# Performance work log

Hardware: AMD Instinct MI355X
Metric: run time of the kernel (lower is better)

## Reference

```python
import jax, jax.numpy as jnp
import numpy as np

R = 32            # voxel resolution
ALPHA = 0.1       # LeakyReLU slope
BN_EPS = 1e-4     # BatchNormalization epsilon
VOX_EPS = 1e-6    # Voxelization eps (normalize=True)


def _bn_train(x, gamma, beta, axes):
    # training-mode batch norm over `axes`, channel axis = 1
    mean = jnp.mean(x, axes, keepdims=True)
    var = jnp.var(x, axes, keepdims=True)
    bshape = (1, -1) + (1,) * (x.ndim - 2)
    return gamma.reshape(bshape) * (x - mean) * jax.lax.rsqrt(var + BN_EPS) + beta.reshape(bshape)


def _lrelu(x):
    return jnp.where(x >= 0, x, ALPHA * x)


def _voxelize(features, coords):
    # features [B,C,N], coords [B,3,N] -> grid [B,C,R,R,R], norm_coords [B,3,N] in [0,R-1]
    centered = coords - jnp.mean(coords, axis=2, keepdims=True)
    max_norm = jnp.max(jnp.linalg.norm(centered, axis=1, keepdims=True), axis=2, keepdims=True)
    norm = centered / (max_norm * 2.0 + VOX_EPS) + 0.5
    norm = jnp.clip(norm * R, 0.0, R - 1)
    vox = jnp.round(norm).astype(jnp.int32)              # [B,3,N]
    flat = (vox[:, 0] * R + vox[:, 1]) * R + vox[:, 2]   # [B,N]

    def per_batch(f, idx):  # f [C,N], idx [N]
        sums = jax.ops.segment_sum(f.T, idx, num_segments=R ** 3)            # [R^3,C]
        cnt = jax.ops.segment_sum(jnp.ones_like(idx, f.dtype), idx, num_segments=R ** 3)
        return (sums / jnp.maximum(cnt, 1.0)[:, None]).T                      # [C,R^3]

    grid = jax.vmap(per_batch)(features, flat)            # [B,C,R^3]
    B, C = features.shape[0], features.shape[1]
    return grid.reshape(B, C, R, R, R), norm


def _conv3d(x, w, b):
    # x [B,C,D,H,W], w [k,k,k,Cin,Cout], 'same' padding
    y = jax.lax.conv_general_dilated(x, w, (1, 1, 1), 'SAME',
                                     dimension_numbers=('NCDHW', 'DHWIO', 'NCDHW'))
    return y + b.reshape(1, -1, 1, 1, 1)


def _trilinear_devoxelize(vf, coords):
    # vf [B,C,R^3], coords [B,3,N] in [0,R-1] -> [B,C,N]
    c0f = jnp.clip(jnp.floor(coords), 0.0, R - 1)
    frac = coords - c0f                                   # [B,3,N]
    c0 = c0f.astype(jnp.int32)
    c1 = jnp.minimum(c0 + 1, R - 1)
    out = jnp.zeros((vf.shape[0], vf.shape[1], coords.shape[2]), vf.dtype)
    for dx in (0, 1):
        for dy in (0, 1):
            for dz in (0, 1):
                xs = c1[:, 0] if dx else c0[:, 0]
                ys = c1[:, 1] if dy else c0[:, 1]
                zs = c1[:, 2] if dz else c0[:, 2]
                w = ((frac[:, 0] if dx else 1 - frac[:, 0]) *
                     (frac[:, 1] if dy else 1 - frac[:, 1]) *
                     (frac[:, 2] if dz else 1 - frac[:, 2]))           # [B,N]
                idx = (xs * R + ys) * R + zs                            # [B,N]
                g = jnp.take_along_axis(vf, idx[:, None, :], axis=2)    # [B,C,N]
                out = out + w[:, None, :] * g
    return out


def setup_inputs() -> dict:
    key = jax.random.key(0)
    ks = jax.random.split(key, 16)
    B, C, N, K = 8, 64, 16384, 3
    s = 0.05
    return {
        'features': jax.random.normal(ks[0], (B, C, N), jnp.float32),
        'coords': jax.random.normal(ks[1], (B, 3, N), jnp.float32),
        'conv1_w': jax.random.normal(ks[2], (K, K, K, C, C), jnp.float32) * s,
        'conv1_b': jnp.zeros((C,), jnp.float32),
        'bn1_gamma': jnp.ones((C,), jnp.float32),
        'bn1_beta': jnp.zeros((C,), jnp.float32),
        'conv2_w': jax.random.normal(ks[3], (K, K, K, C, C), jnp.float32) * s,
        'conv2_b': jnp.zeros((C,), jnp.float32),
        'bn2_gamma': jnp.ones((C,), jnp.float32),
        'bn2_beta': jnp.zeros((C,), jnp.float32),
        'pf_w': jax.random.normal(ks[4], (C, C), jnp.float32) * s,
        'pf_bias': jnp.zeros((C,), jnp.float32),
        'pf_gamma': jnp.ones((C,), jnp.float32),
        'pf_beta': jnp.zeros((C,), jnp.float32),
    }


def reference(features, coords, conv1_w, conv1_b, bn1_gamma, bn1_beta,
              conv2_w, conv2_b, bn2_gamma, bn2_beta,
              pf_w, pf_bias, pf_gamma, pf_beta):
    vgrid, norm_coords = _voxelize(features, coords)
    v = _lrelu(_bn_train(_conv3d(vgrid, conv1_w, conv1_b), bn1_gamma, bn1_beta, (0, 2, 3, 4)))
    v = _lrelu(_bn_train(_conv3d(v, conv2_w, conv2_b), bn2_gamma, bn2_beta, (0, 2, 3, 4)))
    vflat = v.reshape(v.shape[0], v.shape[1], -1)                 # [B,C,R^3]
    vpts = _trilinear_devoxelize(vflat, norm_coords)              # [B,C,N]
    # point branch: shared MLP (1x1 conv) + BN + LeakyReLU
    p = jnp.einsum('bcn,cd->bdn', features, pf_w) + pf_bias[None, :, None]
    p = _lrelu(_bn_train(p, pf_gamma, pf_beta, (0, 2)))
    return vpts + p, coords
```

## Files before the change

### kernel.cpp

```cpp
#include <hip/hip_runtime.h>
#include <stdint.h>

#define RR 32
#define R3 32768
#define NB 8
#define NCH 64
#define NP 16384

typedef unsigned short u16;
typedef uint32_t u32;
typedef __attribute__((ext_vector_type(8))) short bf8;
typedef __attribute__((ext_vector_type(4))) float f4;
typedef __attribute__((ext_vector_type(16))) float f16x;

#define MFMA(a,b,c)   __builtin_amdgcn_mfma_f32_16x16x32_bf16(a,b,c,0,0,0)
#define MFMA32(a,b,c) __builtin_amdgcn_mfma_f32_32x32x16_bf16(a,b,c,0,0,0)

__device__ __forceinline__ float bf2f(u16 v){
  union { u32 u; float f; } x; x.u = ((u32)v) << 16; return x.f;
}
__device__ __forceinline__ float u2f(u32 u){
  union { u32 u; float f; } x; x.u = u; return x.f;
}
__device__ __forceinline__ u16 f2bf(float f){
  union { float f; u32 u; } x; x.f = f;
  u32 r = x.u + 0x7fffu + ((x.u >> 16) & 1u);
  return (u16)(r >> 16);
}
__device__ __forceinline__ float ldf(const void* p, size_t i, int isbf){
  return isbf ? bf2f(((const u16*)p)[i]) : ((const float*)p)[i];
}

#define OFF_GRID  0ull
#define OFF_BUF1  33554432ull
#define OFF_FT    33554432ull
#define OFF_P     67108864ull
#define OFF_CNT   83886080ull
#define OFF_SMALL 84934656ull
#define OFF_STAT  84936704ull
#define OFF_OFFS  84948992ull
#define OFF_NC    85997568ull
#define OFF_VIDX  87570432ull
#define OFF_SORT  88094720ull
#define OFF_WF1   88619008ull
#define OFF_WF2   88840192ull
#define OFF_WFP   89061376ull
#define WS_NEED   89069568ull
#define ZOFF      OFF_CNT
#define ZBYTES    1062912ull

__global__ void k_dtype(const uint32_t* __restrict__ gamma_raw, int* __restrict__ flag){
  if (threadIdx.x == 0) *flag = (gamma_raw[0] == 0x3F800000u) ? 0 : 1;
}

__global__ void k_coordstats(const void* __restrict__ coords, float* __restrict__ small,
                             const int* __restrict__ dflag){
  int b = blockIdx.x; int tid = threadIdx.x;
  int isbf = *dflag;
  __shared__ float red[1024];
  size_t cb = (size_t)b*3*NP;
  float sx=0.f, sy=0.f, sz=0.f;
  for (int n = tid; n < NP; n += 1024){
    sx += ldf(coords, cb+n, isbf);
    sy += ldf(coords, cb+NP+n, isbf);
    sz += ldf(coords, cb+2*NP+n, isbf);
  }
  float m[3]; float* sums[3] = {&sx,&sy,&sz};
  for (int a = 0; a < 3; a++){
    red[tid] = *sums[a]; __syncthreads();
    for (int s = 512; s > 0; s >>= 1){ if (tid < s) red[tid] += red[tid+s]; __syncthreads(); }
    m[a] = red[0] * (1.0f/NP); __syncthreads();
  }
  float vm = 0.f;
  for (int n = tid; n < NP; n += 1024){
    float cx = ldf(coords, cb+n, isbf)      - m[0];
    float cy = ldf(coords, cb+NP+n, isbf)   - m[1];
    float cz = ldf(coords, cb+2*NP+n, isbf) - m[2];
    vm = fmaxf(vm, sqrtf(cx*cx + cy*cy + cz*cz));
  }
  red[tid] = vm; __syncthreads();
  for (int s = 512; s > 0; s >>= 1){ if (tid < s) red[tid] = fmaxf(red[tid], red[tid+s]); __syncthreads(); }
  if (tid == 0){
    small[384 + b*4 + 0] = m[0];
    small[384 + b*4 + 1] = m[1];
    small[384 + b*4 + 2] = m[2];
    small[384 + b*4 + 3] = 1.0f / (2.0f*red[0] + 1e-6f);
  }
}

__global__ void k_pointprep(const void* __restrict__ coords, const float* __restrict__ small,
                            float* __restrict__ nc, int* __restrict__ vidx, int* __restrict__ cnt,
                            const int* __restrict__ dflag){
  int g = blockIdx.x*256 + threadIdx.x;
  int isbf = *dflag;
  int b = g >> 14; int n = g & (NP-1);
  float mx = small[384+b*4+0], my = small[384+b*4+1], mz = small[384+b*4+2], sc = small[384+b*4+3];
  size_t cb = (size_t)b*3*NP;
  float nx = ((ldf(coords, cb+n, isbf)      - mx)*sc + 0.5f) * 32.0f;
  float ny = ((ldf(coords, cb+NP+n, isbf)   - my)*sc + 0.5f) * 32.0f;
  float nz = ((ldf(coords, cb+2*NP+n, isbf) - mz)*sc + 0.5f) * 32.0f;
  nx = fminf(fmaxf(nx, 0.f), 31.f);
  ny = fminf(fmaxf(ny, 0.f), 31.f);
  nz = fminf(fmaxf(nz, 0.f), 31.f);
  nc[(b*3+0)*NP + n] = nx; nc[(b*3+1)*NP + n] = ny; nc[(b*3+2)*NP + n] = nz;
  int vx = (int)rintf(nx), vy = (int)rintf(ny), vz = (int)rintf(nz);
  int flat = (vx*32 + vy)*32 + vz;
  vidx[g] = flat;
  atomicAdd(&cnt[b*R3 + flat], 1);
}

__global__ void k_scan(const int* __restrict__ cnt, int* __restrict__ off){
  __shared__ int part[1024];
  int b = blockIdx.x, tid = threadIdx.x;
  int base = b*R3 + tid*32;
  int s = 0;
  for (int i = 0; i < 32; i++) s += cnt[base + i];
  part[tid] = s; __syncthreads();
  for (int st = 1; st < 1024; st <<= 1){
    int v = (tid >= st) ? part[tid - st] : 0;
    __syncthreads();
    part[tid] += v;
    __syncthreads();
  }
  int run = (tid == 0) ? 0 : part[tid - 1];
  for (int i = 0; i < 32; i++){ off[base + i] = run; run += cnt[base + i]; }
}

__global__ void k_sortpts(const int* __restrict__ vidx, int* __restrict__ off, int* __restrict__ sorted){
  int g = blockIdx.x*256 + threadIdx.x;
  int b = g >> 14; int n = g & (NP-1);
  int v = vidx[g];
  int slot = atomicAdd(&off[b*R3 + v], 1);
  sorted[b*NP + slot] = n;
}

__global__ __launch_bounds__(256) void k_voxsum(const u16* __restrict__ fT, const int* __restrict__ sorted,
                         const int* __restrict__ cnt, const int* __restrict__ off,
                         u16* __restrict__ grid){
  int wid = blockIdx.x*4 + (threadIdx.x >> 6);
  int lane = threadIdx.x & 63;
  int b = wid >> 11;
  int v0 = (wid & 2047) << 4;
  int base = b*R3 + v0;
  int c = 0, e = 0;
  if (lane < 16){ c = cnt[base + lane]; e = off[base + lane]; }
  int start = __shfl(e - c, 0);
  int total = __shfl(e, 15) - start;
  const int* sb = sorted + (size_t)b*NP;
  int sp = 0;
  if (lane < total) sp = sb[start + lane];
  #pragma unroll
  for (int i = 0; i < 16; i++){
    int ci = __shfl(c, i);
    int rel = __shfl(e, i) - ci - start;
    float a0 = 0.f, a1 = 0.f;
    int j = 0;
    for (; j + 1 < ci; j += 2){
      int k0 = rel + j, k1 = k0 + 1;
      int n0 = (k0 < 64) ? __shfl(sp, k0) : sb[start + k0];
      int n1 = (k1 < 64) ? __shfl(sp, k1) : sb[start + k1];
      a0 += bf2f(fT[((size_t)(b*NP + n0))*64 + lane]);
      a1 += bf2f(fT[((size_t)(b*NP + n1))*64 + lane]);
    }
    if (j < ci){
      int k0 = rel + j;
      int n0 = (k0 < 64) ? __shfl(sp, k0) : sb[start + k0];
      a0 += bf2f(fT[((size_t)(b*NP + n0))*64 + lane]);
    }
    float acc = a0 + a1;
    grid[((size_t)(base + i))*64 + lane] = f2bf(acc / (float)max(ci, 1));
  }
}

__global__ void k_wprep(const void* __restrict__ w, u16* __restrict__ wfrag, const int* __restrict__ dflag){
  int idx = blockIdx.x; int lane = threadIdx.x;
  int isbf = *dflag;
  int ntl = idx & 3; int kk = (idx >> 2) & 1; int tap = idx >> 3;
  int lh = lane & 15, quad = lane >> 4;
  int n = ntl*16 + lh;
  u16* dst = wfrag + ((size_t)idx*64 + lane)*8;
  for (int j = 0; j < 8; j++){
    int k = kk*32 + quad*8 + j;
    dst[j] = f2bf(ldf(w, (size_t)(tap*64 + k)*64 + n, isbf));
  }
}

__global__ void k_wprep32(const void* __restrict__ w, u16* __restrict__ wfrag, const int* __restrict__ dflag){
  int idx = blockIdx.x; int lane = threadIdx.x;
  int isbf = *dflag;
  int nh = idx & 1; int ks = (idx >> 1) & 3; int tap = idx >> 3;
  int n = nh*32 + (lane & 31);
  int khalf = lane >> 5;
  u16* dst = wfrag + ((size_t)idx*64 + lane)*8;
  for (int j = 0; j < 8; j++){
    int cin = ks*16 + khalf*8 + j;
    dst[j] = f2bf(ldf(w, (size_t)(tap*64 + cin)*64 + n, isbf));
  }
}

__device__ __forceinline__ void bn_params(const float* __restrict__ spread, int c, float invM,
                                          float* mean, float* rs){
  float su = 0.f, sq = 0.f;
  #pragma unroll
  for (int i = 0; i < 8; i++){ su += spread[i*128 + c]; sq += spread[i*128 + 64 + c]; }
  float m = su * invM;
  *mean = m;
  *rs = rsqrtf(sq*invM - m*m + 1e-4f);
}

#define ISSUE_W(BANK, TAP) do { \
  _Pragma("unroll") \
  for (int ks_ = 0; ks_ < 4; ks_++) \
    BANK[ks_] = *(const bf8*)(wstream + (size_t)((TAP)*4 + ks_)*1024); \
} while(0)

#define ISSUE_A8(BANK, TAP, H) do { \
  const int t_ = (TAP); \
  const int dwi_ = t_ % 3, dvi_ = (t_/3) % 3, dui_ = t_/9; \
  const u16* rp0_ = &lds_in[((2*(H) + dui_)*6 + vsel + dvi_)*2176]; \
  const u16* rp1_ = rp0_ + 6*2176; \
  const int wp_ = mlane + dwi_; \
  const int wb_ = wp_*64, wx_ = wp_ & 7; \
  _Pragma("unroll") \
  for (int ks_ = 0; ks_ < 4; ks_++){ \
    const int off_ = wb_ + ((((ks_*2) + khalf) ^ wx_) << 3); \
    BANK[ks_]     = *(const bf8*)(rp0_ + off_); \
    BANK[4 + ks_] = *(const bf8*)(rp1_ + off_); \
  } \
} while(0)

#define CONSUME(BW, BA, ACC0, ACC1) do { \
  _Pragma("unroll") \
  for (int ks_ = 0; ks_ < 4; ks_++){ \
    ACC0 = MFMA32(BA[ks_],     BW[ks_], ACC0); \
    ACC1 = MFMA32(BA[4 + ks_], BW[ks_], ACC1); \
  } \
} while(0)

template<int BN>
__global__ __launch_bounds__(512, 1) void k_conv_t(const u16* __restrict__ in, const u16* __restrict__ wfrag,
                                                   u16* __restrict__ out, const float* __restrict__ spread,
                                                   const void* __restrict__ gamma, const void* __restrict__ beta,
                                                   const int* __restrict__ dflag){
  __shared__ u16 lds_in[36*2176];
  __shared__ float bnA[64], bnB[64];
  int bx = blockIdx.x;
  int b = bx >> 6; int r = bx & 63;
  int u0 = (r >> 3) * 4; int v0 = (r & 7) * 4;
  int tid = threadIdx.x, wv = tid >> 6, lane = tid & 63;

  if constexpr (BN){
    if (tid < 64){
      int isbf = *dflag;
      float mean, rs;
      bn_params(spread, tid, 1.0f/(NB*R3), &mean, &rs);
      float ga = ldf(gamma, tid, isbf), be = ldf(beta, tid, isbf);
      float A = ga*rs;
      bnA[tid] = A; bnB[tid] = be - mean*A;
    }
    __syncthreads();
  }

  uint4 zz; zz.x = 0; zz.y = 0; zz.z = 0; zz.w = 0;
  for (int ri = wv; ri < 36; ri += 8){
    int u2 = u0 + (ri / 6) - 1;
    int v2 = v0 + (ri % 6) - 1;
    uint4* dstrow = (uint4*)&lds_in[ri*2176];
    if ((unsigned)u2 > 31u || (unsigned)v2 > 31u){
      for (int i = lane; i < 272; i += 64) dstrow[i] = zz;
      continue;
    }
    const uint4* src = (const uint4*)(in + ((size_t)(b*R3 + (u2*32 + v2)*32))*64);
    if (lane < 8) dstrow[lane] = zz;
    else if (lane < 16) dstrow[264 + (lane & 7)] = zz;
    #pragma unroll
    for (int ch = 0; ch < 4; ch++){
      int idx = ch*64 + lane;
      int w = idx >> 3, cc = idx & 7;
      uint4 v = src[idx];
      if constexpr (BN){
        u32 in4[4] = {v.x, v.y, v.z, v.w};
        u32 o4[4];
        #pragma unroll
        for (int k = 0; k < 4; k++){
          int c = cc*8 + 2*k;
          float lo = u2f(in4[k] << 16);
          float hi = u2f(in4[k] & 0xFFFF0000u);
          lo = bnA[c]*lo + bnB[c];     lo = (lo >= 0.f) ? lo : 0.1f*lo;
          hi = bnA[c+1]*hi + bnB[c+1]; hi = (hi >= 0.f) ? hi : 0.1f*hi;
          o4[k] = (u32)f2bf(lo) | ((u32)f2bf(hi) << 16);
        }
        v.x = o4[0]; v.y = o4[1]; v.z = o4[2]; v.w = o4[3];
      }
      int wp = w + 1;
      dstrow[wp*8 + (cc ^ (wp & 7))] = v;
    }
  }
  __syncthreads();

  int vsel = wv & 3, nh = wv >> 2;
  int v_i = v0 + vsel;
  int mlane = lane & 31;
  int khalf = lane >> 5;
  f16x acc0, acc1, acc2, acc3;
  #pragma unroll
  for (int i = 0; i < 16; i++){ acc0[i] = 0.f; acc1[i] = 0.f; acc2[i] = 0.f; acc3[i] = 0.f; }

  const u16* wstream = wfrag + (size_t)nh*512 + (size_t)lane*8;

  bf8 W0[4], W1[4], W2[4];
  bf8 Aa[8], Ab[8];

  ISSUE_W(W0, 0);
  ISSUE_W(W1, 1);
  ISSUE_A8(Aa, 0, 0);

  #pragma unroll
  for (int tap = 0; tap < 27; ++tap){
    const int pf = tap + 2;
    if (pf < 27){
      if (pf % 3 == 0)      ISSUE_W(W0, pf);
      else if (pf % 3 == 1) ISSUE_W(W1, pf);
      else                  ISSUE_W(W2, pf);
    }
    ISSUE_A8(Ab, tap, 1);
    __builtin_amdgcn_sched_barrier(0);
    if (tap < 25)       asm volatile("s_waitcnt vmcnt(8) lgkmcnt(8)");
    else if (tap == 25) asm volatile("s_waitcnt vmcnt(4) lgkmcnt(8)");
    else                asm volatile("s_waitcnt vmcnt(0) lgkmcnt(8)");
    __builtin_amdgcn_sched_barrier(0);
    {
      const int wsel = tap % 3;
      if (wsel == 0)      CONSUME(W0, Aa, acc0, acc1);
      else if (wsel == 1) CONSUME(W1, Aa, acc0, acc1);
      else                CONSUME(W2, Aa, acc0, acc1);
    }
    if (tap + 1 < 27) ISSUE_A8(Aa, tap + 1, 0);
    __builtin_amdgcn_sched_barrier(0);
    if (tap < 25)       asm volatile("s_waitcnt vmcnt(8) lgkmcnt(8)");
    else if (tap == 25) asm volatile("s_waitcnt vmcnt(4) lgkmcnt(8)");
    else                asm volatile("s_waitcnt vmcnt(0) lgkmcnt(0)");
    __builtin_amdgcn_sched_barrier(0);
    {
      const int wsel = tap % 3;
      if (wsel == 0)      CONSUME(W0, Ab, acc2, acc3);
      else if (wsel == 1) CONSUME(W1, Ab, acc2, acc3);
      else                CONSUME(W2, Ab, acc2, acc3);
    }
  }

  int co = nh*32 + mlane;
  int rbase = 4*khalf;
  size_t base0 = ((size_t)(b*R3 + ((u0+0)*32 + v_i)*32))*64;
  size_t base1 = ((size_t)(b*R3 + ((u0+1)*32 + v_i)*32))*64;
  size_t base2 = ((size_t)(b*R3 + ((u0+2)*32 + v_i)*32))*64;
  size_t base3 = ((size_t)(b*R3 + ((u0+3)*32 + v_i)*32))*64;
  #pragma unroll
  for (int reg = 0; reg < 16; reg++){
    int row = (reg & 3) + 8*(reg >> 2) + rbase;
    out[base0 + (size_t)row*64 + co] = f2bf(acc0[reg]);
    out[base1 + (size_t)row*64 + co] = f2bf(acc1[reg]);
    out[base2 + (size_t)row*64 + co] = f2bf(acc2[reg]);
    out[base3 + (size_t)row*64 + co] = f2bf(acc3[reg]);
  }
}

__global__ __launch_bounds__(256) void k_stats2(const u16* __restrict__ buf, float* __restrict__ spread, int M){
  __shared__ float sred[4*128];
  int tid = threadIdx.x, bx = blockIdx.x;
  int wv = tid >> 6, lane = tid & 63;
  int sub = lane & 7;
  int g = bx*256 + tid;
  float s[8], s2[8];
  #pragma unroll
  for (int j = 0; j < 8; j++){ s[j] = 0.f; s2[j] = 0.f; }
  const uint4* p4 = (const uint4*)buf;
  size_t total = (size_t)M * 8;
  for (size_t f = g; f < total; f += 262144){
    uint4 v = p4[f];
    u32 ws_[4] = {v.x, v.y, v.z, v.w};
    #pragma unroll
    for (int k = 0; k < 4; k++){
      float lo = u2f(ws_[k] << 16);
      float hi = u2f(ws_[k] & 0xFFFF0000u);
      s[2*k]   += lo; s2[2*k]   += lo*lo;
      s[2*k+1] += hi; s2[2*k+1] += hi*hi;
    }
  }
  #pragma unroll
  for (int j = 0; j < 8; j++){
    #pragma unroll
    for (int m = 8; m <= 32; m <<= 1){
      s[j]  += __shfl_xor(s[j],  m);
      s2[j] += __shfl_xor(s2[j], m);
    }
  }
  if (lane < 8){
    #pragma unroll
    for (int j = 0; j < 8; j++){
      sred[wv*128 + sub*8 + j]      = s[j];
      sred[wv*128 + 64 + sub*8 + j] = s2[j];
    }
  }
  __syncthreads();
  if (tid < 128){
    float t = sred[tid] + sred[128+tid] + sred[256+tid] + sred[384+tid];
    atomicAdd(&spread[(bx & 7)*128 + tid], t);
  }
}

__global__ __launch_bounds__(256) void k_ftrans(const void* __restrict__ feat, u16* __restrict__ fT,
                                                const int* __restrict__ dflag){
  __shared__ u16 t[64*72];
  int bx = blockIdx.x;
  int isbf = *dflag;
  int b = bx >> 8; int n0 = (bx & 255) * 64;
  int tid = threadIdx.x;
  int c = tid >> 2, q = tid & 3;
  if (isbf){
    const uint4* src = (const uint4*)((const u16*)feat + ((size_t)(b*NCH + c))*NP + n0 + q*16);
    uint4 v0 = src[0], v1 = src[1];
    *(uint4*)&t[c*72 + q*16]     = v0;
    *(uint4*)&t[c*72 + q*16 + 8] = v1;
  } else {
    const float4* src = (const float4*)((const float*)feat + ((size_t)(b*NCH + c))*NP + n0 + q*16);
    #pragma unroll
    for (int h = 0; h < 4; h++){
      float4 f = src[h];
      u16* d = &t[c*72 + q*16 + h*4];
      d[0] = f2bf(f.x); d[1] = f2bf(f.y); d[2] = f2bf(f.z); d[3] = f2bf(f.w);
    }
  }
  __syncthreads();
  int n = tid >> 2, qc = tid & 3;
  union { u16 h[16]; uint4 v[2]; } pk;
  #pragma unroll
  for (int j = 0; j < 16; j++) pk.h[j] = t[(qc*16 + j)*72 + n];
  uint4* dst = (uint4*)(fT + ((size_t)(b*NP + n0 + n))*64 + qc*16);
  dst[0] = pk.v[0]; dst[1] = pk.v[1];
}

__global__ void k_pgemm(const u16* __restrict__ fT, const u16* __restrict__ wfp, u16* __restrict__ p){
  __shared__ u16 As[128*64];
  int bx = blockIdx.x;
  size_t row0 = (size_t)bx * 128;
  int tid = threadIdx.x, wv = tid >> 6, lane = tid & 63;
  const uint4* src = (const uint4*)(fT + row0*64);
  uint4* dst = (uint4*)As;
  for (int i = tid; i < 1024; i += 256) dst[i] = src[i];
  __syncthreads();
  int lh = lane & 15, quad = lane >> 4;
  f4 z4 = {0.f,0.f,0.f,0.f};
  f4 acc[2][4];
  for (int i = 0; i < 2; i++) for (int j = 0; j < 4; j++) acc[i][j] = z4;
  const u16* ap = &As[(wv*32)*64];
  #pragma unroll
  for (int kk = 0; kk < 2; kk++){
    bf8 a0 = *(const bf8*)(ap + lh*64 + kk*32 + quad*8);
    bf8 a1 = *(const bf8*)(ap + (16+lh)*64 + kk*32 + quad*8);
    #pragma unroll
    for (int ntl = 0; ntl < 4; ntl++){
      bf8 bf = *(const bf8*)(wfp + ((size_t)(kk*4 + ntl)*64 + lane)*8);
      acc[0][ntl] = MFMA(a0, bf, acc[0][ntl]);
      acc[1][ntl] = MFMA(a1, bf, acc[1][ntl]);
    }
  }
  #pragma unroll
  for (int mt = 0; mt < 2; mt++)
    for (int ntl = 0; ntl < 4; ntl++)
      for (int reg = 0; reg < 4; reg++){
        int rr = wv*32 + mt*16 + quad*4 + reg;
        p[(row0 + rr)*64 + ntl*16 + lh] = f2bf(acc[mt][ntl][reg]);
      }
}

__global__ void k_devox(const u16* __restrict__ grid, const u16* __restrict__ p,
                        const float* __restrict__ stP, const float* __restrict__ st2,
                        const void* __restrict__ pfg, const void* __restrict__ pfb,
                        const void* __restrict__ g2, const void* __restrict__ b2,
                        const float* __restrict__ nc, void* __restrict__ out0,
                        const int* __restrict__ dflag){
  __shared__ float t[64*65];
  int bx = blockIdx.x;
  int isbf = *dflag;
  int b = bx >> 8; int n0 = (bx & 255) * 64;
  int tid = threadIdx.x, wv = tid >> 6, lane = tid & 63;
  int c = lane;
  float meanP, rsP;
  bn_params(stP, c, 1.0f/(NB*NP), &meanP, &rsP);
  float gaP = ldf(pfg, c, isbf), beP = ldf(pfb, c, isbf);
  float mean2, rs2;
  bn_params(st2, c, 1.0f/(NB*R3), &mean2, &rs2);
  float ga2 = ldf(g2, c, isbf), be2 = ldf(b2, c, isbf);
  float A2 = ga2*rs2, B2 = be2 - mean2*A2;
  for (int pt = wv; pt < 64; pt += 4){
    int n = n0 + pt;
    float nx = nc[(b*3+0)*NP + n];
    float ny = nc[(b*3+1)*NP + n];
    float nz = nc[(b*3+2)*NP + n];
    float x0f = floorf(nx), y0f = floorf(ny), z0f = floorf(nz);
    int x0 = (int)x0f, y0 = (int)y0f, z0 = (int)z0f;
    float fx = nx - x0f, fy = ny - y0f, fz = nz - z0f;
    int x1 = min(x0+1,31), y1 = min(y0+1,31), z1 = min(z0+1,31);
    float acc = 0.f;
    #pragma unroll
    for (int k = 0; k < 8; k++){
      int dx = k >> 2, dy = (k >> 1) & 1, dz = k & 1;
      int xs = dx ? x1 : x0, ys = dy ? y1 : y0, zs = dz ? z1 : z0;
      float wgt = (dx ? fx : 1.f-fx)*(dy ? fy : 1.f-fy)*(dz ? fz : 1.f-fz);
      float gv = bf2f(grid[((size_t)(b*R3 + (xs*32+ys)*32 + zs))*64 + c]);
      gv = A2*gv + B2;
      gv = (gv >= 0.f) ? gv : 0.1f*gv;
      acc += wgt * gv;
    }
    float pv = bf2f(p[((size_t)(b*NP + n))*64 + c]);
    float y = gaP*(pv - meanP)*rsP + beP;
    y = (y >= 0.f) ? y : 0.1f*y;
    t[pt*65 + c] = acc + y;
  }
  __syncthreads();
  for (int cp = 0; cp < 16; cp++){
    int co = wv + cp*4;
    size_t oi = ((size_t)(b*NCH + co))*NP + n0 + lane;
    float val = t[lane*65 + co];
    if (isbf) ((u16*)out0)[oi] = f2bf(val);
    else      ((float*)out0)[oi] = val;
  }
}

__global__ void k_copycoords(const void* __restrict__ coords, void* __restrict__ out0,
                             const int* __restrict__ dflag){
  int g = blockIdx.x*256 + threadIdx.x;
  int isbf = *dflag;
  size_t oi = (size_t)NB*NCH*NP + g;
  if (isbf) ((u16*)out0)[oi]   = ((const u16*)coords)[g];
  else      ((float*)out0)[oi] = ((const float*)coords)[g];
}

extern "C" void kernel_launch(void* const* d_in, const int* in_sizes, int n_in,
                              void* d_out, int out_size, void* d_ws, size_t ws_size,
                              hipStream_t stream){
  if (ws_size < WS_NEED) return;

  const void* feat   = d_in[0];
  const void* coords = d_in[1];
  const void* w1     = d_in[2];
  const void* g1     = d_in[4];
  const void* b1     = d_in[5];
  const void* w2     = d_in[6];
  const void* g2     = d_in[8];
  const void* b2     = d_in[9];
  const void* pw     = d_in[10];
  const void* pg     = d_in[12];
  const void* pb     = d_in[13];

  char* ws = (char*)d_ws;
  u16*   gridv = (u16*)(ws + OFF_GRID);
  u16*   buf1  = (u16*)(ws + OFF_BUF1);
  u16*   fT    = (u16*)(ws + OFF_FT);
  u16*   p     = (u16*)(ws + OFF_P);
  int*   cnt   = (int*)(ws + OFF_CNT);
  float* small = (float*)(ws + OFF_SMALL);
  int*   dflag = (int*)(small + 448);
  float* stat  = (float*)(ws + OFF_STAT);
  int*   offs  = (int*)(ws + OFF_OFFS);
  float* nc    = (float*)(ws + OFF_NC);
  int*   vidx  = (int*)(ws + OFF_VIDX);
  int*   sorted= (int*)(ws + OFF_SORT);
  u16*   wf1   = (u16*)(ws + OFF_WF1);
  u16*   wf2   = (u16*)(ws + OFF_WF2);
  u16*   wfp   = (u16*)(ws + OFF_WFP);

  hipMemsetAsync(ws + ZOFF, 0, ZBYTES, stream);
  k_dtype<<<1, 64, 0, stream>>>((const uint32_t*)g1, dflag);

  k_wprep32<<<27*8, 64, 0, stream>>>(w1, wf1, dflag);
  k_wprep32<<<27*8, 64, 0, stream>>>(w2, wf2, dflag);
  k_wprep<<<8, 64, 0, stream>>>(pw, wfp, dflag);

  k_coordstats<<<NB, 1024, 0, stream>>>(coords, small, dflag);
  k_pointprep<<<NB*NP/256, 256, 0, stream>>>(coords, small, nc, vidx, cnt, dflag);
  k_scan<<<NB, 1024, 0, stream>>>(cnt, offs);
  k_sortpts<<<NB*NP/256, 256, 0, stream>>>(vidx, offs, sorted);

  k_ftrans<<<NB*NP/64, 256, 0, stream>>>(feat, fT, dflag);
  k_voxsum<<<NB*R3/64, 256, 0, stream>>>(fT, sorted, cnt, offs, gridv);
  k_pgemm<<<NB*NP/128, 256, 0, stream>>>(fT, wfp, p);
  k_stats2<<<1024, 256, 0, stream>>>(p, stat + 2048, NB*NP);

  k_conv_t<0><<<NB*64, 512, 0, stream>>>(gridv, wf1, buf1, nullptr, nullptr, nullptr, nullptr);
  k_stats2<<<1024, 256, 0, stream>>>(buf1, stat + 0, NB*R3);

  k_conv_t<1><<<NB*64, 512, 0, stream>>>(buf1, wf2, gridv, stat + 0, g1, b1, dflag);
  k_stats2<<<1024, 256, 0, stream>>>(gridv, stat + 1024, NB*R3);

  k_devox<<<NB*NP/64, 256, 0, stream>>>(gridv, p, stat + 2048, stat + 1024,
                                        pg, pb, g2, b2, nc, d_out, dflag);
  k_copycoords<<<NB*3*NP/256, 256, 0, stream>>>(coords, d_out, dflag);
}
```

Baseline: 391.4 us.

## Fuse BN statistics into conv epilogues and coords copy into pointprep

The conv kernels now reduce per-channel sum and sum-of-squares from their fp32 accumulators and atomically add them into a spread stats buffer. This removes the two separate k_stats2 passes that reread each conv output from memory. The coordinate passthrough copy moves into k_pointprep, which drops one more launch. Statistics now come from fp32 values rather than bf16-rounded outputs, and the added atomics could contend on the 8-way spread slots.

```diff
diff --git a/kernel.cpp b/kernel.cpp
--- a/kernel.cpp
+++ b/kernel.cpp
@@ -90,12 +90,20 @@
 
 __global__ void k_pointprep(const void* __restrict__ coords, const float* __restrict__ small,
                             float* __restrict__ nc, int* __restrict__ vidx, int* __restrict__ cnt,
-                            const int* __restrict__ dflag){
+                            void* __restrict__ out0, const int* __restrict__ dflag){
   int g = blockIdx.x*256 + threadIdx.x;
   int isbf = *dflag;
   int b = g >> 14; int n = g & (NP-1);
   float mx = small[384+b*4+0], my = small[384+b*4+1], mz = small[384+b*4+2], sc = small[384+b*4+3];
   size_t cb = (size_t)b*3*NP;
+  size_t ob = (size_t)NB*NCH*NP + cb + n;
+  if (isbf){
+    const u16* cs = (const u16*)coords; u16* o = (u16*)out0;
+    o[ob] = cs[cb+n]; o[ob+NP] = cs[cb+NP+n]; o[ob+2*NP] = cs[cb+2*NP+n];
+  } else {
+    const float* cs = (const float*)coords; float* o = (float*)out0;
+    o[ob] = cs[cb+n]; o[ob+NP] = cs[cb+NP+n]; o[ob+2*NP] = cs[cb+2*NP+n];
+  }
   float nx = ((ldf(coords, cb+n, isbf)      - mx)*sc + 0.5f) * 32.0f;
   float ny = ((ldf(coords, cb+NP+n, isbf)   - my)*sc + 0.5f) * 32.0f;
   float nz = ((ldf(coords, cb+2*NP+n, isbf) - mz)*sc + 0.5f) * 32.0f;
@@ -240,6 +248,7 @@
 template<int BN>
 __global__ __launch_bounds__(512, 1) void k_conv_t(const u16* __restrict__ in, const u16* __restrict__ wfrag,
                                                    u16* __restrict__ out, const float* __restrict__ spread,
+                                                   float* __restrict__ statOut,
                                                    const void* __restrict__ gamma, const void* __restrict__ beta,
                                                    const int* __restrict__ dflag){
   __shared__ u16 lds_in[36*2176];
@@ -362,6 +371,20 @@
     out[base1 + (size_t)row*64 + co] = f2bf(acc1[reg]);
     out[base2 + (size_t)row*64 + co] = f2bf(acc2[reg]);
     out[base3 + (size_t)row*64 + co] = f2bf(acc3[reg]);
+  }
+
+  float s = 0.f, s2 = 0.f;
+  #pragma unroll
+  for (int reg = 0; reg < 16; reg++){
+    float v0_ = acc0[reg], v1_ = acc1[reg], v2_ = acc2[reg], v3_ = acc3[reg];
+    s  += v0_ + v1_ + v2_ + v3_;
+    s2 += v0_*v0_ + v1_*v1_ + v2_*v2_ + v3_*v3_;
+  }
+  s  += __shfl_xor(s, 32);
+  s2 += __shfl_xor(s2, 32);
+  if (lane < 32){
+    atomicAdd(&statOut[(bx & 7)*128 + co], s);
+    atomicAdd(&statOut[(bx & 7)*128 + 64 + co], s2);
   }
 }
 
@@ -528,15 +551,6 @@
   }
 }
 
-__global__ void k_copycoords(const void* __restrict__ coords, void* __restrict__ out0,
-                             const int* __restrict__ dflag){
-  int g = blockIdx.x*256 + threadIdx.x;
-  int isbf = *dflag;
-  size_t oi = (size_t)NB*NCH*NP + g;
-  if (isbf) ((u16*)out0)[oi]   = ((const u16*)coords)[g];
-  else      ((float*)out0)[oi] = ((const float*)coords)[g];
-}
-
 extern "C" void kernel_launch(void* const* d_in, const int* in_sizes, int n_in,
                               void* d_out, int out_size, void* d_ws, size_t ws_size,
                               hipStream_t stream){
@@ -579,7 +593,7 @@
   k_wprep<<<8, 64, 0, stream>>>(pw, wfp, dflag);
 
   k_coordstats<<<NB, 1024, 0, stream>>>(coords, small, dflag);
-  k_pointprep<<<NB*NP/256, 256, 0, stream>>>(coords, small, nc, vidx, cnt, dflag);
+  k_pointprep<<<NB*NP/256, 256, 0, stream>>>(coords, small, nc, vidx, cnt, d_out, dflag);
   k_scan<<<NB, 1024, 0, stream>>>(cnt, offs);
   k_sortpts<<<NB*NP/256, 256, 0, stream>>>(vidx, offs, sorted);
 
@@ -588,13 +602,9 @@
   k_pgemm<<<NB*NP/128, 256, 0, stream>>>(fT, wfp, p);
   k_stats2<<<1024, 256, 0, stream>>>(p, stat + 2048, NB*NP);
 
-  k_conv_t<0><<<NB*64, 512, 0, stream>>>(gridv, wf1, buf1, nullptr, nullptr, nullptr, nullptr);
-  k_stats2<<<1024, 256, 0, stream>>>(buf1, stat + 0, NB*R3);
-
-  k_conv_t<1><<<NB*64, 512, 0, stream>>>(buf1, wf2, gridv, stat + 0, g1, b1, dflag);
-  k_stats2<<<1024, 256, 0, stream>>>(gridv, stat + 1024, NB*R3);
+  k_conv_t<0><<<NB*64, 512, 0, stream>>>(gridv, wf1, buf1, nullptr, stat + 0, nullptr, nullptr, nullptr);
+  k_conv_t<1><<<NB*64, 512, 0, stream>>>(buf1, wf2, gridv, stat + 0, stat + 1024, g1, b1, dflag);
 
   k_devox<<<NB*NP/64, 256, 0, stream>>>(gridv, p, stat + 2048, stat + 1024,
                                         pg, pb, g2, b2, nc, d_out, dflag);
-  k_copycoords<<<NB*3*NP/256, 256, 0, stream>>>(coords, d_out, dflag);
-}
+}
```

After: 370.1 us. 5.4% less time.
